# Kernel optimization log

Measured on AMD Instinct MI355X. Metric: run time of the kernel, lower is better.

The kernel has to match this reference:

```python
import jax, jax.numpy as jnp
import numpy as np

SEQ = 2048
D_MODEL = 2048
N_HEAD = 16
D_QK = 128
D_V = 128
THETA = 10000.0


def setup_inputs() -> dict:
    key = jax.random.key(0)
    kx, kq, kk, kv, ko = jax.random.split(key, 5)
    x = jax.random.normal(kx, (SEQ, D_MODEL), dtype=jnp.float32)
    q = jax.random.normal(kq, (N_HEAD, D_MODEL, D_QK), dtype=jnp.float32)
    k = jax.random.normal(kk, (N_HEAD, D_MODEL, D_QK), dtype=jnp.float32)
    v = jax.random.normal(kv, (N_HEAD, D_MODEL, D_V), dtype=jnp.float32)
    o = jax.random.normal(ko, (N_HEAD, D_V, D_MODEL), dtype=jnp.float32)
    theta_factor = jnp.asarray(THETA, dtype=jnp.float32)
    return {"x": x, "q": q, "k": k, "v": v, "o": o, "theta_factor": theta_factor}


def _rope_embed(x, d_qk, theta_factor):
    # x: [..., S, d]. Rotate-half RoPE with frequencies theta^(-i/d_rope),
    # then scale by d_qk^(-1/4) so q.k gets the usual 1/sqrt(d_qk).
    S, d = x.shape[-2], x.shape[-1]
    d_rope = d // 2
    rates = theta_factor ** (-jnp.arange(d_rope, dtype=x.dtype) / d_rope)  # [d_rope]
    ang = jnp.arange(S, dtype=x.dtype)[:, None] * rates[None, :]           # [S, d_rope]
    sin, cos = jnp.sin(ang), jnp.cos(ang)
    x1, x2 = x[..., :d_rope], x[..., d_rope:]
    y = jnp.concatenate([cos * x1 - sin * x2, sin * x1 + cos * x2], axis=-1)
    return y * (d_qk ** -0.25)


def reference(x, q, k, v, o, theta_factor):
    # x: [S, D]; q,k: [H, D, d_qk]; v: [H, D, d_v]; o: [H, d_v, D]
    S = x.shape[0]
    d_qk = q.shape[2]
    qs = jnp.einsum('sd,hde->hse', x, q)   # [H, S, d_qk]
    ks = jnp.einsum('sd,hde->hse', x, k)   # [H, S, d_qk]
    vs = jnp.einsum('sd,hde->hse', x, v)   # [H, S, d_v]
    rq = _rope_embed(qs, d_qk, theta_factor)
    rk = _rope_embed(ks, d_qk, theta_factor)
    scores = jnp.einsum('hse,hte->hst', rq, rk)  # [H, S, S]
    causal = jnp.tril(jnp.ones((S, S), dtype=bool))
    scores = jnp.where(causal[None], scores, -jnp.inf)
    w = jax.nn.softmax(scores, axis=-1)
    y = jnp.einsum('hst,hte->hse', w, vs)        # [H, S, d_v]
    z = jnp.einsum('hse,hed->sd', y, o)          # [S, D] (sum over heads)
    return z
```

## Files before the change

### kernel.cpp

```cpp
#include <hip/hip_runtime.h>
#include <hip/hip_bf16.h>

#define SEQ 2048
#define DM  2048
#define NH  16
#define DE  128
#define DR  64
#define LDT 72
#define LDK 136

typedef __attribute__((ext_vector_type(8))) short bf16x8;
typedef __attribute__((ext_vector_type(4))) float f32x4;

__device__ __forceinline__ unsigned short f2bf(float f) {
  unsigned u = __float_as_uint(f);
  u += 0x7fff + ((u >> 16) & 1);
  return (unsigned short)(u >> 16);
}
__device__ __forceinline__ float bf2f(unsigned short h) {
  return __uint_as_float((unsigned)h << 16);
}

__device__ __forceinline__ void gld16(const unsigned short* g, unsigned short* l) {
  __builtin_amdgcn_global_load_lds(
      (const __attribute__((address_space(1))) unsigned int*)g,
      (__attribute__((address_space(3))) unsigned int*)l, 16, 0, 0);
}

__global__ void k_split(const float* __restrict__ in, unsigned short* __restrict__ hi,
                        unsigned short* __restrict__ lo, int n4) {
  int i = blockIdx.x * blockDim.x + threadIdx.x;
  int stride = gridDim.x * blockDim.x;
  for (int idx = i; idx < n4; idx += stride) {
    float4 v = ((const float4*)in)[idx];
    ushort4 h, l;
    h.x = f2bf(v.x); l.x = f2bf(v.x - bf2f(h.x));
    h.y = f2bf(v.y); l.y = f2bf(v.y - bf2f(h.y));
    h.z = f2bf(v.z); l.z = f2bf(v.z - bf2f(h.z));
    h.w = f2bf(v.w); l.w = f2bf(v.w - bf2f(h.w));
    ((ushort4*)hi)[idx] = h;
    ((ushort4*)lo)[idx] = l;
  }
}

__global__ void k_prep_qkv(const float* __restrict__ q, const float* __restrict__ k,
                           const float* __restrict__ v,
                           unsigned short* __restrict__ wqh, unsigned short* __restrict__ wql,
                           unsigned short* __restrict__ wkh, unsigned short* __restrict__ wkl,
                           unsigned short* __restrict__ wvh) {
  __shared__ float tile[32][33];
  int z = blockIdx.z;
  int which = z >> 4, h = z & 15;
  const float* in = (which == 0) ? q : (which == 1) ? k : v;
  size_t bo = (size_t)h * DM * DE;
  int r0 = blockIdx.y * 32, c0 = blockIdx.x * 32;
  int tx = threadIdx.x, ty = threadIdx.y;
  #pragma unroll
  for (int i = 0; i < 32; i += 8)
    tile[ty + i][tx] = in[bo + (size_t)(r0 + ty + i) * DE + (c0 + tx)];
  __syncthreads();
  #pragma unroll
  for (int i = 0; i < 32; i += 8) {
    float vv = tile[tx][ty + i];
    unsigned short hh = f2bf(vv);
    size_t oidx = bo + (size_t)(c0 + ty + i) * DM + (r0 + tx);
    if (which == 0)      { wqh[oidx] = hh; wql[oidx] = f2bf(vv - bf2f(hh)); }
    else if (which == 1) { wkh[oidx] = hh; wkl[oidx] = f2bf(vv - bf2f(hh)); }
    else                 { wvh[oidx] = hh; }
  }
}

__global__ void k_transpose_one(const float* __restrict__ in, unsigned short* __restrict__ out,
                                int rows, int cols) {
  __shared__ float tile[32][33];
  size_t bo = (size_t)blockIdx.z * rows * cols;
  int r0 = blockIdx.y * 32, c0 = blockIdx.x * 32;
  int tx = threadIdx.x, ty = threadIdx.y;
  #pragma unroll
  for (int i = 0; i < 32; i += 8)
    tile[ty + i][tx] = in[bo + (size_t)(r0 + ty + i) * cols + (c0 + tx)];
  __syncthreads();
  #pragma unroll
  for (int i = 0; i < 32; i += 8)
    out[bo + (size_t)(c0 + ty + i) * rows + (r0 + tx)] = f2bf(tile[tx][ty + i]);
}

__global__ void k_rope_tables(const float* __restrict__ theta_p,
                              float* __restrict__ cost, float* __restrict__ sint) {
  int s = blockIdx.x, j = threadIdx.x;
  float theta = theta_p[0];
  float rate = powf(theta, -(float)j * (1.0f / (float)DR));
  float ang = (float)s * rate;
  cost[s * DR + j] = cosf(ang);
  sint[s * DR + j] = sinf(ang);
}

__launch_bounds__(256)
__global__ void k_projall(const unsigned short* __restrict__ xh, const unsigned short* __restrict__ xl,
                          const unsigned short* __restrict__ wqh, const unsigned short* __restrict__ wql,
                          const unsigned short* __restrict__ wkh, const unsigned short* __restrict__ wkl,
                          const unsigned short* __restrict__ wvh,
                          unsigned short* __restrict__ rqh, unsigned short* __restrict__ rql,
                          unsigned short* __restrict__ rkh, unsigned short* __restrict__ rkl,
                          unsigned short* __restrict__ vstt,
                          const float* __restrict__ cost, const float* __restrict__ sint) {
  __shared__ unsigned short Ahs[2][128 * 32];
  __shared__ unsigned short Als[2][128 * 32];
  __shared__ unsigned short Bhs[2][128 * 32];
  __shared__ unsigned short Bls[2][128 * 32];
  int mt = blockIdx.x;
  int mat = blockIdx.y >> 4, h = blockIdx.y & 15;
  bool split = (mat < 2);
  const unsigned short* wph = (mat == 0 ? wqh : (mat == 1 ? wkh : wvh)) + (size_t)h * DE * DM;
  const unsigned short* wpl = (mat == 0 ? wql : wkl) + (size_t)h * DE * DM;
  int m0 = mt * 128;
  int tid = threadIdx.x, lane = tid & 63, wid = tid >> 6;
  int wr = wid >> 1, wc = wid & 1;

  f32x4 zero = {0.f, 0.f, 0.f, 0.f};
  f32x4 acc[4][4];
  #pragma unroll
  for (int i = 0; i < 4; ++i)
    #pragma unroll
    for (int j = 0; j < 4; ++j) acc[i][j] = zero;

  auto STAGE = [&](int buf, int k0) {
    #pragma unroll
    for (int p = 0; p < 2; ++p) {
      int r = p * 64 + wid * 16 + (lane >> 2);
      int c = ((lane & 3) ^ ((r >> 1) & 3)) * 8;
      int ld = r * 32 + (lane & 3) * 8;
      gld16(&xh[(size_t)(m0 + r) * DM + k0 + c], &Ahs[buf][ld]);
      gld16(&wph[(size_t)r * DM + k0 + c], &Bhs[buf][ld]);
      if (split) {
        gld16(&xl[(size_t)(m0 + r) * DM + k0 + c], &Als[buf][ld]);
        gld16(&wpl[(size_t)r * DM + k0 + c], &Bls[buf][ld]);
      }
    }
  };

  const int NT = DM / 32;
  STAGE(0, 0);
  int cl_ = lane & 15;
  int chunk = lane >> 4;
  #pragma unroll 2
  for (int t = 0; t < NT; ++t) {
    int buf = t & 1;
    __syncthreads();
    if (t + 1 < NT) STAGE(buf ^ 1, (t + 1) * 32);
    bf16x8 ah[4], al[4], bh[4], bl[4];
    #pragma unroll
    for (int mf = 0; mf < 4; ++mf) {
      int row = wr * 64 + mf * 16 + cl_;
      int off = row * 32 + ((chunk ^ ((row >> 1) & 3)) * 8);
      ah[mf] = *(const bf16x8*)&Ahs[buf][off];
      if (split) al[mf] = *(const bf16x8*)&Als[buf][off];
    }
    #pragma unroll
    for (int nf = 0; nf < 4; ++nf) {
      int nfi = wc * 2 + (nf & 1) + (nf >> 1) * 4;
      int row = nfi * 16 + cl_;
      int off = row * 32 + ((chunk ^ ((row >> 1) & 3)) * 8);
      bh[nf] = *(const bf16x8*)&Bhs[buf][off];
      if (split) bl[nf] = *(const bf16x8*)&Bls[buf][off];
    }
    if (split) {
      #pragma unroll
      for (int mf = 0; mf < 4; ++mf)
        #pragma unroll
        for (int nf = 0; nf < 4; ++nf) {
          acc[mf][nf] = __builtin_amdgcn_mfma_f32_16x16x32_bf16(ah[mf], bh[nf], acc[mf][nf], 0, 0, 0);
          acc[mf][nf] = __builtin_amdgcn_mfma_f32_16x16x32_bf16(al[mf], bh[nf], acc[mf][nf], 0, 0, 0);
          acc[mf][nf] = __builtin_amdgcn_mfma_f32_16x16x32_bf16(ah[mf], bl[nf], acc[mf][nf], 0, 0, 0);
        }
    } else {
      #pragma unroll
      for (int mf = 0; mf < 4; ++mf)
        #pragma unroll
        for (int nf = 0; nf < 4; ++nf)
          acc[mf][nf] = __builtin_amdgcn_mfma_f32_16x16x32_bf16(ah[mf], bh[nf], acc[mf][nf], 0, 0, 0);
    }
  }

  int cl = lane & 15, rl = (lane >> 4) * 4;
  if (mat == 2) {
    #pragma unroll
    for (int mf = 0; mf < 4; ++mf)
      #pragma unroll
      for (int nf = 0; nf < 4; ++nf) {
        int nfi = wc * 2 + (nf & 1) + (nf >> 1) * 4;
        #pragma unroll
        for (int j = 0; j < 4; ++j) {
          int s = m0 + wr * 64 + mf * 16 + rl + j;
          int e = nfi * 16 + cl;
          vstt[((size_t)h * DE + e) * SEQ + s] = f2bf(acc[mf][nf][j]);
        }
      }
  } else {
    unsigned short* oh = (mat == 0) ? rqh : rkh;
    unsigned short* ol = (mat == 0) ? rql : rkl;
    const float qsc = 0.2973017787506803f;
    #pragma unroll
    for (int mf = 0; mf < 4; ++mf)
      #pragma unroll
      for (int nf = 0; nf < 2; ++nf)
        #pragma unroll
        for (int j = 0; j < 4; ++j) {
          int s = m0 + wr * 64 + mf * 16 + rl + j;
          int e = wc * 32 + (nf & 1) * 16 + cl;
          float x1 = acc[mf][nf][j];
          float x2 = acc[mf][nf + 2][j];
          float c  = cost[s * DR + e];
          float sn = sint[s * DR + e];
          float v1 = (c * x1 - sn * x2) * qsc;
          float v2 = (sn * x1 + c * x2) * qsc;
          size_t i1 = ((size_t)h * SEQ + s) * DE + e;
          size_t i2 = i1 + DR;
          unsigned short h1 = f2bf(v1), h2 = f2bf(v2);
          oh[i1] = h1; ol[i1] = f2bf(v1 - bf2f(h1));
          oh[i2] = h2; ol[i2] = f2bf(v2 - bf2f(h2));
        }
  }
}

#define LOADKV(t0)                                                        \
  pkh0 = *(const int4*)&Kh[(size_t)((t0) + sk_r     ) * DE + sk_c];       \
  pkh1 = *(const int4*)&Kh[(size_t)((t0) + sk_r + 16) * DE + sk_c];       \
  pkh2 = *(const int4*)&Kh[(size_t)((t0) + sk_r + 32) * DE + sk_c];       \
  pkh3 = *(const int4*)&Kh[(size_t)((t0) + sk_r + 48) * DE + sk_c];       \
  pkl0 = *(const int4*)&Kl[(size_t)((t0) + sk_r     ) * DE + sk_c];       \
  pkl1 = *(const int4*)&Kl[(size_t)((t0) + sk_r + 16) * DE + sk_c];       \
  pkl2 = *(const int4*)&Kl[(size_t)((t0) + sk_r + 32) * DE + sk_c];       \
  pkl3 = *(const int4*)&Kl[(size_t)((t0) + sk_r + 48) * DE + sk_c];       \
  pvv0 = *(const int4*)&Vt[(size_t)(sv_r     ) * SEQ + (t0) + sv_c];      \
  pvv1 = *(const int4*)&Vt[(size_t)(sv_r + 32) * SEQ + (t0) + sv_c];      \
  pvv2 = *(const int4*)&Vt[(size_t)(sv_r + 64) * SEQ + (t0) + sv_c];      \
  pvv3 = *(const int4*)&Vt[(size_t)(sv_r + 96) * SEQ + (t0) + sv_c];

#define STOREKV()                                                         \
  *(int4*)&Khi[(sk_r     ) * LDK + sk_c] = pkh0;                          \
  *(int4*)&Khi[(sk_r + 16) * LDK + sk_c] = pkh1;                          \
  *(int4*)&Khi[(sk_r + 32) * LDK + sk_c] = pkh2;                          \
  *(int4*)&Khi[(sk_r + 48) * LDK + sk_c] = pkh3;                          \
  *(int4*)&Klo[(sk_r     ) * LDK + sk_c] = pkl0;                          \
  *(int4*)&Klo[(sk_r + 16) * LDK + sk_c] = pkl1;                          \
  *(int4*)&Klo[(sk_r + 32) * LDK + sk_c] = pkl2;                          \
  *(int4*)&Klo[(sk_r + 48) * LDK + sk_c] = pkl3;                          \
  *(int4*)&Vtl[(sv_r     ) * LDT + sv_c] = pvv0;                          \
  *(int4*)&Vtl[(sv_r + 32) * LDT + sv_c] = pvv1;                          \
  *(int4*)&Vtl[(sv_r + 64) * LDT + sv_c] = pvv2;                          \
  *(int4*)&Vtl[(sv_r + 96) * LDT + sv_c] = pvv3;

__launch_bounds__(256, 2)
__global__ void k_attn(const unsigned short* __restrict__ rqh, const unsigned short* __restrict__ rql,
                       const unsigned short* __restrict__ rkh, const unsigned short* __restrict__ rkl,
                       const unsigned short* __restrict__ vstt,
                       unsigned short* __restrict__ yb) {
  __shared__ unsigned short Khi[64 * LDK];
  __shared__ unsigned short Klo[64 * LDK];
  __shared__ unsigned short Vtl[128 * LDT];
  __shared__ unsigned short Pl[64 * LDT];
  int bid = blockIdx.x;
  int g = bid >> 4;
  int qt = (g < 16) ? (31 - g) : (g - 16);
  int h  = bid & 15;
  int m0 = qt * 64;
  int tid = threadIdx.x, lane = tid & 63, wid = tid >> 6;
  const unsigned short* Qh = rqh + (size_t)h * SEQ * DE;
  const unsigned short* Ql = rql + (size_t)h * SEQ * DE;
  const unsigned short* Kh = rkh + (size_t)h * SEQ * DE;
  const unsigned short* Kl = rkl + (size_t)h * SEQ * DE;
  const unsigned short* Vt = vstt + (size_t)h * DE * SEQ;
  int cl = lane & 15, hi = lane >> 4;

  bf16x8 qfh[4], qfl[4];
  {
    int qrow = m0 + wid * 16 + cl;
    #pragma unroll
    for (int ks = 0; ks < 4; ++ks) {
      qfh[ks] = *(const bf16x8*)&Qh[(size_t)qrow * DE + ks * 32 + hi * 8];
      qfl[ks] = *(const bf16x8*)&Ql[(size_t)qrow * DE + ks * 32 + hi * 8];
    }
  }

  f32x4 zero = {0.f, 0.f, 0.f, 0.f};
  f32x4 acc[8];
  #pragma unroll
  for (int nf = 0; nf < 8; ++nf) acc[nf] = zero;
  float mrow[4], lrow[4];
  #pragma unroll
  for (int j = 0; j < 4; ++j) { mrow[j] = -3e38f; lrow[j] = 0.f; }

  int sk_r = tid >> 4, sk_c = (tid & 15) * 8;
  int sv_r = tid >> 3, sv_c = (tid & 7) * 8;

  int4 pkh0, pkh1, pkh2, pkh3, pkl0, pkl1, pkl2, pkl3, pvv0, pvv1, pvv2, pvv3;

  int ntiles = qt + 1;
  LOADKV(0)
  for (int t = 0; t < ntiles; ++t) {
    int t0 = t * 64;
    STOREKV()
    __syncthreads();
    if (t + 1 < ntiles) { LOADKV(t0 + 64) }

    f32x4 sacc[4];
    #pragma unroll
    for (int tf = 0; tf < 4; ++tf) sacc[tf] = zero;
    __builtin_amdgcn_s_setprio(1);
    #pragma unroll
    for (int ks = 0; ks < 4; ++ks) {
      int kk = ks * 32 + hi * 8;
      #pragma unroll
      for (int tf = 0; tf < 4; ++tf) {
        int r = (tf * 16 + cl) * LDK + kk;
        bf16x8 bh = *(const bf16x8*)&Khi[r];
        bf16x8 bl = *(const bf16x8*)&Klo[r];
        sacc[tf] = __builtin_amdgcn_mfma_f32_16x16x32_bf16(qfh[ks], bh, sacc[tf], 0, 0, 0);
        sacc[tf] = __builtin_amdgcn_mfma_f32_16x16x32_bf16(qfl[ks], bh, sacc[tf], 0, 0, 0);
        sacc[tf] = __builtin_amdgcn_mfma_f32_16x16x32_bf16(qfh[ks], bl, sacc[tf], 0, 0, 0);
      }
    }
    __builtin_amdgcn_s_setprio(0);
    if (t == ntiles - 1) {
      int sb = m0 + wid * 16 + hi * 4;
      #pragma unroll
      for (int tf = 0; tf < 4; ++tf) {
        int tc = t0 + tf * 16 + cl;
        #pragma unroll
        for (int j = 0; j < 4; ++j)
          if (tc > sb + j) sacc[tf][j] = -3e38f;
      }
    }
    #pragma unroll
    for (int j = 0; j < 4; ++j) {
      float mx = fmaxf(fmaxf(sacc[0][j], sacc[1][j]), fmaxf(sacc[2][j], sacc[3][j]));
      mx = fmaxf(mx, __shfl_xor(mx, 1));
      mx = fmaxf(mx, __shfl_xor(mx, 2));
      mx = fmaxf(mx, __shfl_xor(mx, 4));
      mx = fmaxf(mx, __shfl_xor(mx, 8));
      float mnew = fmaxf(mrow[j], mx);
      float sc = __expf(mrow[j] - mnew);
      float sum = 0.f;
      #pragma unroll
      for (int tf = 0; tf < 4; ++tf) {
        float p = __expf(sacc[tf][j] - mnew);
        sacc[tf][j] = p;
        sum += p;
      }
      sum += __shfl_xor(sum, 1);
      sum += __shfl_xor(sum, 2);
      sum += __shfl_xor(sum, 4);
      sum += __shfl_xor(sum, 8);
      lrow[j] = lrow[j] * sc + sum;
      mrow[j] = mnew;
      #pragma unroll
      for (int nf = 0; nf < 8; ++nf) acc[nf][j] *= sc;
    }
    #pragma unroll
    for (int tf = 0; tf < 4; ++tf)
      #pragma unroll
      for (int j = 0; j < 4; ++j)
        Pl[(wid * 16 + hi * 4 + j) * LDT + tf * 16 + cl] = f2bf(sacc[tf][j]);
    __builtin_amdgcn_s_setprio(1);
    #pragma unroll
    for (int ks = 0; ks < 2; ++ks) {
      int kk = ks * 32 + hi * 8;
      bf16x8 a = *(const bf16x8*)&Pl[(wid * 16 + cl) * LDT + kk];
      #pragma unroll
      for (int nf = 0; nf < 8; ++nf) {
        bf16x8 b = *(const bf16x8*)&Vtl[(nf * 16 + cl) * LDT + kk];
        acc[nf] = __builtin_amdgcn_mfma_f32_16x16x32_bf16(a, b, acc[nf], 0, 0, 0);
      }
    }
    __builtin_amdgcn_s_setprio(0);
    __syncthreads();
  }

  #pragma unroll
  for (int j = 0; j < 4; ++j) {
    float inv = 1.0f / lrow[j];
    #pragma unroll
    for (int nf = 0; nf < 8; ++nf) acc[nf][j] *= inv;
  }
  #pragma unroll
  for (int nf = 0; nf < 8; ++nf)
    #pragma unroll
    for (int j = 0; j < 4; ++j) {
      int s = m0 + wid * 16 + hi * 4 + j;
      int e = nf * 16 + cl;
      yb[(size_t)s * DM + h * DE + e] = f2bf(acc[nf][j]);
    }
}

__launch_bounds__(256)
__global__ void k_out(const unsigned short* __restrict__ yb,
                      const unsigned short* __restrict__ otb,
                      float* __restrict__ z) {
  __shared__ unsigned short Ahs[2][128 * 32];
  __shared__ unsigned short Bhs[2][128 * 32];
  int m0 = blockIdx.x * 128, n0 = blockIdx.y * 128;
  int tid = threadIdx.x, lane = tid & 63, wid = tid >> 6;
  int wr = wid >> 1, wc = wid & 1;
  f32x4 zero = {0.f, 0.f, 0.f, 0.f};
  f32x4 acc[4][4];
  #pragma unroll
  for (int i = 0; i < 4; ++i)
    #pragma unroll
    for (int j = 0; j < 4; ++j) acc[i][j] = zero;

  auto STAGE = [&](int buf, int k0) {
    #pragma unroll
    for (int p = 0; p < 2; ++p) {
      int r = p * 64 + wid * 16 + (lane >> 2);
      int c = ((lane & 3) ^ ((r >> 1) & 3)) * 8;
      int ld = r * 32 + (lane & 3) * 8;
      gld16(&yb[(size_t)(m0 + r) * DM + k0 + c], &Ahs[buf][ld]);
      gld16(&otb[(size_t)(n0 + r) * DM + k0 + c], &Bhs[buf][ld]);
    }
  };

  const int NT = DM / 32;
  STAGE(0, 0);
  int cl_ = lane & 15;
  int chunk = lane >> 4;
  #pragma unroll 2
  for (int t = 0; t < NT; ++t) {
    int buf = t & 1;
    __syncthreads();
    if (t + 1 < NT) STAGE(buf ^ 1, (t + 1) * 32);
    bf16x8 a[4], b[4];
    #pragma unroll
    for (int mf = 0; mf < 4; ++mf) {
      int row = wr * 64 + mf * 16 + cl_;
      a[mf] = *(const bf16x8*)&Ahs[buf][row * 32 + ((chunk ^ ((row >> 1) & 3)) * 8)];
    }
    #pragma unroll
    for (int nf = 0; nf < 4; ++nf) {
      int nfi = wc * 2 + (nf & 1) + (nf >> 1) * 4;
      int row = nfi * 16 + cl_;
      b[nf] = *(const bf16x8*)&Bhs[buf][row * 32 + ((chunk ^ ((row >> 1) & 3)) * 8)];
    }
    #pragma unroll
    for (int mf = 0; mf < 4; ++mf)
      #pragma unroll
      for (int nf = 0; nf < 4; ++nf)
        acc[mf][nf] = __builtin_amdgcn_mfma_f32_16x16x32_bf16(a[mf], b[nf], acc[mf][nf], 0, 0, 0);
  }
  int cl = lane & 15, rl = (lane >> 4) * 4;
  #pragma unroll
  for (int mf = 0; mf < 4; ++mf)
    #pragma unroll
    for (int nf = 0; nf < 4; ++nf) {
      int nfi = wc * 2 + (nf & 1) + (nf >> 1) * 4;
      #pragma unroll
      for (int j = 0; j < 4; ++j) {
        int s = m0 + wr * 64 + mf * 16 + rl + j;
        int d = n0 + nfi * 16 + cl;
        z[(size_t)s * DM + d] = acc[mf][nf][j];
      }
    }
}

extern "C" void kernel_launch(void* const* d_in, const int* in_sizes, int n_in,
                              void* d_out, int out_size, void* d_ws, size_t ws_size,
                              hipStream_t stream) {
  const float* x  = (const float*)d_in[0];
  const float* q  = (const float*)d_in[1];
  const float* k  = (const float*)d_in[2];
  const float* v  = (const float*)d_in[3];
  const float* o  = (const float*)d_in[4];
  const float* th = (const float*)d_in[5];
  float* z = (float*)d_out;
  char* ws = (char*)d_ws;
  const size_t MB = 1024 * 1024;
  unsigned short* xh  = (unsigned short*)(ws);
  unsigned short* xl  = (unsigned short*)(ws + 8 * MB);
  unsigned short* wqh = (unsigned short*)(ws + 16 * MB);
  unsigned short* wql = (unsigned short*)(ws + 24 * MB);
  unsigned short* wkh = (unsigned short*)(ws + 32 * MB);
  unsigned short* wkl = (unsigned short*)(ws + 40 * MB);
  unsigned short* wvh = (unsigned short*)(ws + 48 * MB);
  unsigned short* rqh = (unsigned short*)(ws + 56 * MB);
  unsigned short* rql = (unsigned short*)(ws + 64 * MB);
  unsigned short* rkh = (unsigned short*)(ws + 72 * MB);
  unsigned short* rkl = (unsigned short*)(ws + 80 * MB);
  unsigned short* vst = (unsigned short*)(ws + 88 * MB);
  float* cost = (float*)(ws + 96 * MB);
  float* sint = (float*)(ws + 96 * MB + 512 * 1024);
  unsigned short* yb  = (unsigned short*)(ws + 16 * MB);
  unsigned short* otb = (unsigned short*)(ws + 24 * MB);

  dim3 tb(32, 8);
  k_rope_tables<<<SEQ, DR, 0, stream>>>(th, cost, sint);
  k_split<<<2048, 256, 0, stream>>>(x, xh, xl, SEQ * DM / 4);
  k_prep_qkv<<<dim3(DE / 32, DM / 32, 48), tb, 0, stream>>>(q, k, v, wqh, wql, wkh, wkl, wvh);
  k_projall<<<dim3(16, 48), 256, 0, stream>>>(xh, xl, wqh, wql, wkh, wkl, wvh,
                                              rqh, rql, rkh, rkl, vst, cost, sint);
  k_transpose_one<<<dim3(DM / 32, (NH * DE) / 32, 1), tb, 0, stream>>>(o, otb, NH * DE, DM);
  k_attn<<<512, 256, 0, stream>>>(rqh, rql, rkh, rkl, vst, yb);
  k_out<<<dim3(16, 16), 256, 0, stream>>>(yb, otb, z);
}
```

Before: 314.1 us.

## Merge weight prep kernels and add lazy softmax rescaling in attention

Folds the o-weight transpose into the q/k/v weight prep kernel so it runs as one launch, moving the o buffer to its own workspace region so it no longer aliases wq. In the attention loop, the running max is only updated and the accumulator only rescaled when some row's tile max exceeds the stored max by more than 8. Otherwise exponentials are taken against the stale max, which skips the per-tile rescale of the accumulators. Values up to about e^8 stay well within fp32 range, but the bf16 P values lose some relative precision.

Result: no change. 312.3 us (-0.6%).

```diff
diff --git a/kernel.cpp b/kernel.cpp
--- a/kernel.cpp
+++ b/kernel.cpp
@@ -43,46 +43,47 @@
   }
 }
 
-__global__ void k_prep_qkv(const float* __restrict__ q, const float* __restrict__ k,
-                           const float* __restrict__ v,
+__global__ void k_prep_all(const float* __restrict__ q, const float* __restrict__ k,
+                           const float* __restrict__ v, const float* __restrict__ o,
                            unsigned short* __restrict__ wqh, unsigned short* __restrict__ wql,
                            unsigned short* __restrict__ wkh, unsigned short* __restrict__ wkl,
-                           unsigned short* __restrict__ wvh) {
+                           unsigned short* __restrict__ wvh, unsigned short* __restrict__ otb) {
   __shared__ float tile[32][33];
-  int z = blockIdx.z;
-  int which = z >> 4, h = z & 15;
-  const float* in = (which == 0) ? q : (which == 1) ? k : v;
-  size_t bo = (size_t)h * DM * DE;
-  int r0 = blockIdx.y * 32, c0 = blockIdx.x * 32;
+  int f = blockIdx.x;
   int tx = threadIdx.x, ty = threadIdx.y;
-  #pragma unroll
-  for (int i = 0; i < 32; i += 8)
-    tile[ty + i][tx] = in[bo + (size_t)(r0 + ty + i) * DE + (c0 + tx)];
-  __syncthreads();
-  #pragma unroll
-  for (int i = 0; i < 32; i += 8) {
-    float vv = tile[tx][ty + i];
-    unsigned short hh = f2bf(vv);
-    size_t oidx = bo + (size_t)(c0 + ty + i) * DM + (r0 + tx);
-    if (which == 0)      { wqh[oidx] = hh; wql[oidx] = f2bf(vv - bf2f(hh)); }
-    else if (which == 1) { wkh[oidx] = hh; wkl[oidx] = f2bf(vv - bf2f(hh)); }
-    else                 { wvh[oidx] = hh; }
-  }
-}
-
-__global__ void k_transpose_one(const float* __restrict__ in, unsigned short* __restrict__ out,
-                                int rows, int cols) {
-  __shared__ float tile[32][33];
-  size_t bo = (size_t)blockIdx.z * rows * cols;
-  int r0 = blockIdx.y * 32, c0 = blockIdx.x * 32;
-  int tx = threadIdx.x, ty = threadIdx.y;
-  #pragma unroll
-  for (int i = 0; i < 32; i += 8)
-    tile[ty + i][tx] = in[bo + (size_t)(r0 + ty + i) * cols + (c0 + tx)];
-  __syncthreads();
-  #pragma unroll
-  for (int i = 0; i < 32; i += 8)
-    out[bo + (size_t)(c0 + ty + i) * rows + (r0 + tx)] = f2bf(tile[tx][ty + i]);
+  if (f < 12288) {
+    int z = f >> 8;
+    int rem = f & 255;
+    int ry = rem >> 2, rx = rem & 3;
+    int which = z >> 4, h = z & 15;
+    const float* in = (which == 0) ? q : (which == 1) ? k : v;
+    size_t bo = (size_t)h * DM * DE;
+    int r0 = ry * 32, c0 = rx * 32;
+    #pragma unroll
+    for (int i = 0; i < 32; i += 8)
+      tile[ty + i][tx] = in[bo + (size_t)(r0 + ty + i) * DE + (c0 + tx)];
+    __syncthreads();
+    #pragma unroll
+    for (int i = 0; i < 32; i += 8) {
+      float vv = tile[tx][ty + i];
+      unsigned short hh = f2bf(vv);
+      size_t oidx = bo + (size_t)(c0 + ty + i) * DM + (r0 + tx);
+      if (which == 0)      { wqh[oidx] = hh; wql[oidx] = f2bf(vv - bf2f(hh)); }
+      else if (which == 1) { wkh[oidx] = hh; wkl[oidx] = f2bf(vv - bf2f(hh)); }
+      else                 { wvh[oidx] = hh; }
+    }
+  } else {
+    int rem = f - 12288;
+    int ry = rem >> 6, rx = rem & 63;
+    int r0 = ry * 32, c0 = rx * 32;
+    #pragma unroll
+    for (int i = 0; i < 32; i += 8)
+      tile[ty + i][tx] = o[(size_t)(r0 + ty + i) * DM + (c0 + tx)];
+    __syncthreads();
+    #pragma unroll
+    for (int i = 0; i < 32; i += 8)
+      otb[(size_t)(c0 + ty + i) * DM + (r0 + tx)] = f2bf(tile[tx][ty + i]);
+  }
 }
 
 __global__ void k_rope_tables(const float* __restrict__ theta_p,
@@ -332,6 +333,7 @@
           if (tc > sb + j) sacc[tf][j] = -3e38f;
       }
     }
+    float mxa[4];
     #pragma unroll
     for (int j = 0; j < 4; ++j) {
       float mx = fmaxf(fmaxf(sacc[0][j], sacc[1][j]), fmaxf(sacc[2][j], sacc[3][j]));
@@ -339,23 +341,47 @@
       mx = fmaxf(mx, __shfl_xor(mx, 2));
       mx = fmaxf(mx, __shfl_xor(mx, 4));
       mx = fmaxf(mx, __shfl_xor(mx, 8));
-      float mnew = fmaxf(mrow[j], mx);
-      float sc = __expf(mrow[j] - mnew);
-      float sum = 0.f;
-      #pragma unroll
-      for (int tf = 0; tf < 4; ++tf) {
-        float p = __expf(sacc[tf][j] - mnew);
-        sacc[tf][j] = p;
-        sum += p;
-      }
-      sum += __shfl_xor(sum, 1);
-      sum += __shfl_xor(sum, 2);
-      sum += __shfl_xor(sum, 4);
-      sum += __shfl_xor(sum, 8);
-      lrow[j] = lrow[j] * sc + sum;
-      mrow[j] = mnew;
-      #pragma unroll
-      for (int nf = 0; nf < 8; ++nf) acc[nf][j] *= sc;
+      mxa[j] = mx;
+    }
+    bool need = (mxa[0] > mrow[0] + 8.f) || (mxa[1] > mrow[1] + 8.f) ||
+                (mxa[2] > mrow[2] + 8.f) || (mxa[3] > mrow[3] + 8.f);
+    if (__any(need)) {
+      #pragma unroll
+      for (int j = 0; j < 4; ++j) {
+        float mnew = fmaxf(mrow[j], mxa[j]);
+        float sc = __expf(mrow[j] - mnew);
+        float sum = 0.f;
+        #pragma unroll
+        for (int tf = 0; tf < 4; ++tf) {
+          float p = __expf(sacc[tf][j] - mnew);
+          sacc[tf][j] = p;
+          sum += p;
+        }
+        sum += __shfl_xor(sum, 1);
+        sum += __shfl_xor(sum, 2);
+        sum += __shfl_xor(sum, 4);
+        sum += __shfl_xor(sum, 8);
+        lrow[j] = lrow[j] * sc + sum;
+        mrow[j] = mnew;
+        #pragma unroll
+        for (int nf = 0; nf < 8; ++nf) acc[nf][j] *= sc;
+      }
+    } else {
+      #pragma unroll
+      for (int j = 0; j < 4; ++j) {
+        float sum = 0.f;
+        #pragma unroll
+        for (int tf = 0; tf < 4; ++tf) {
+          float p = __expf(sacc[tf][j] - mrow[j]);
+          sacc[tf][j] = p;
+          sum += p;
+        }
+        sum += __shfl_xor(sum, 1);
+        sum += __shfl_xor(sum, 2);
+        sum += __shfl_xor(sum, 4);
+        sum += __shfl_xor(sum, 8);
+        lrow[j] += sum;
+      }
     }
     #pragma unroll
     for (int tf = 0; tf < 4; ++tf)
@@ -488,16 +514,15 @@
   unsigned short* vst = (unsigned short*)(ws + 88 * MB);
   float* cost = (float*)(ws + 96 * MB);
   float* sint = (float*)(ws + 96 * MB + 512 * 1024);
+  unsigned short* otb = (unsigned short*)(ws + 98 * MB);
   unsigned short* yb  = (unsigned short*)(ws + 16 * MB);
-  unsigned short* otb = (unsigned short*)(ws + 24 * MB);
 
   dim3 tb(32, 8);
   k_rope_tables<<<SEQ, DR, 0, stream>>>(th, cost, sint);
   k_split<<<2048, 256, 0, stream>>>(x, xh, xl, SEQ * DM / 4);
-  k_prep_qkv<<<dim3(DE / 32, DM / 32, 48), tb, 0, stream>>>(q, k, v, wqh, wql, wkh, wkl, wvh);
+  k_prep_all<<<16384, tb, 0, stream>>>(q, k, v, o, wqh, wql, wkh, wkl, wvh, otb);
   k_projall<<<dim3(16, 48), 256, 0, stream>>>(xh, xl, wqh, wql, wkh, wkl, wvh,
                                               rqh, rql, rkh, rkl, vst, cost, sint);
-  k_transpose_one<<<dim3(DM / 32, (NH * DE) / 32, 1), tb, 0, stream>>>(o, otb, NH * DE, DM);
   k_attn<<<512, 256, 0, stream>>>(rqh, rql, rkh, rkl, vst, yb);
   k_out<<<dim3(16, 16), 256, 0, stream>>>(yb, otb, z);
 }
```
